# Optimization experiments

Hardware: AMD Instinct MI355X
Metric: run time of the kernel (lower is better)

## Reference

```python
import jax, jax.numpy as jnp
import numpy as np

N_HEADS, D_MODEL, D_HEAD = 16, 1024, 64
INIT_STD = 0.02


def setup_inputs() -> dict:
    key = jax.random.key(0)
    ks = jax.random.split(key, 5)
    x = jax.random.normal(ks[0], (4, 2048, D_MODEL), dtype=jnp.float32)
    W_Q = jax.random.normal(ks[1], (N_HEADS, D_MODEL, D_HEAD), dtype=jnp.float32) * INIT_STD
    W_K = jax.random.normal(ks[2], (N_HEADS, D_MODEL, D_HEAD), dtype=jnp.float32) * INIT_STD
    W_V = jax.random.normal(ks[3], (N_HEADS, D_MODEL, D_HEAD), dtype=jnp.float32) * INIT_STD
    W_O = jax.random.normal(ks[4], (N_HEADS, D_HEAD, D_MODEL), dtype=jnp.float32) * INIT_STD
    b_Q = jnp.zeros((N_HEADS, D_HEAD), dtype=jnp.float32)
    b_K = jnp.zeros((N_HEADS, D_HEAD), dtype=jnp.float32)
    b_V = jnp.zeros((N_HEADS, D_HEAD), dtype=jnp.float32)
    b_O = jnp.zeros((D_MODEL,), dtype=jnp.float32)
    return {"normalized_resid_pre": x, "W_Q": W_Q, "W_K": W_K, "W_V": W_V,
            "W_O": W_O, "b_Q": b_Q, "b_K": b_K, "b_V": b_V, "b_O": b_O}


def reference(normalized_resid_pre, W_Q, W_K, W_V, W_O, b_Q, b_K, b_V, b_O):
    x = normalized_resid_pre  # [b, s, d_model]
    q = jnp.einsum('bsm,hmd->bshd', x, W_Q) + b_Q  # [b, s, h, d_head]
    k = jnp.einsum('bsm,hmd->bshd', x, W_K) + b_K
    v = jnp.einsum('bsm,hmd->bshd', x, W_V) + b_V
    scores = jnp.einsum('bqhd,bkhd->bhqk', q, k) / jnp.sqrt(jnp.float32(D_HEAD))
    S = x.shape[1]
    causal = jnp.tril(jnp.ones((S, S), dtype=bool))  # keep key_pos <= query_pos
    scores = jnp.where(causal, scores, jnp.finfo(scores.dtype).min)
    pattern = jax.nn.softmax(scores, axis=-1)  # [b, h, q, k]
    z = jnp.einsum('bhqk,bkhd->bqhd', pattern, v)
    attn_out = jnp.einsum('bqhd,hdm->bqm', z, W_O) + b_O
    return attn_out
```

## Files before the change

### kernel.cpp

```cpp
#include <hip/hip_runtime.h>
#include <hip/hip_bf16.h>
#include <math.h>

typedef __bf16 bf16_t;
typedef bf16_t bf16x8 __attribute__((ext_vector_type(8)));
typedef float f32x4 __attribute__((ext_vector_type(4)));

#define BB 4
#define SS 2048
#define HH 16
#define DMODEL 1024
#define DHEAD 64

#define QSCALE 0.18033688011112042f

__device__ inline unsigned short f2bf(float f) {
    union { __hip_bfloat16 h; unsigned short u; } cvt;
    cvt.h = __float2bfloat16(f);
    return cvt.u;
}

__device__ __forceinline__ void gll16(const unsigned short* g, unsigned short* l) {
    __builtin_amdgcn_global_load_lds(
        (const __attribute__((address_space(1))) unsigned int*)(g),
        (__attribute__((address_space(3))) unsigned int*)(l), 16, 0, 0);
}


__global__ void pack_x(const float* __restrict__ x, unsigned short* __restrict__ xb) {
    int i = blockIdx.x * 256 + threadIdx.x;
    const float4 v = ((const float4*)x)[i];
    unsigned short o[4] = { f2bf(v.x), f2bf(v.y), f2bf(v.z), f2bf(v.w) };
    *(uint2*)(xb + 4 * (size_t)i) = *(uint2*)o;
}

__global__ void pack_wqkv(const float* __restrict__ wq, const float* __restrict__ wk,
                          const float* __restrict__ wv, unsigned short* __restrict__ out) {
    int idx = blockIdx.x * 256 + threadIdx.x;
    int k  = idx & 1023;
    int n  = idx >> 10;
    int mat = n >> 10;
    int n1 = n & 1023;
    int h = n1 >> 6, d = n1 & 63;
    const float* w = (mat == 0) ? wq : (mat == 1) ? wk : wv;
    out[idx] = f2bf(w[(h << 16) + (k << 6) + d]);
}

__global__ void pack_wo(const float* __restrict__ wo, unsigned short* __restrict__ out) {
    int idx = blockIdx.x * 256 + threadIdx.x;
    int k = idx & 1023, n = idx >> 10;
    out[idx] = f2bf(wo[(k << 10) + n]);
}


template <bool SWAP>
__device__ __forceinline__ void mf16(f32x4& d, bf16x8 a, bf16x8 b) {
    if constexpr (SWAP)
        d = __builtin_amdgcn_mfma_f32_16x16x32_bf16(b, a, d, 0, 0, 0);
    else
        d = __builtin_amdgcn_mfma_f32_16x16x32_bf16(a, b, d, 0, 0, 0);
}

#define GBAR()   __builtin_amdgcn_s_barrier()
#define SCHEDB() __builtin_amdgcn_sched_barrier(0)
#define WLGKM0() asm volatile("s_waitcnt lgkmcnt(0)" ::: "memory")

__device__ __forceinline__ void stage2(const unsigned short* g, unsigned short* lb,
                                       int T, int w) {
    const unsigned short* s = g + T * 64;
    gll16(s, lb + w * 8 * 64);
    gll16(s + 64 * 1024, lb + (64 + w * 8) * 64);
}

template <bool SWAP>
__device__ __forceinline__ void ktstep(
    unsigned short (*Ac)[64], unsigned short (*Bc)[64],
    unsigned short (*An)[64], unsigned short (*Bn)[64],
    const unsigned short* gA0, const unsigned short* gA1,
    const unsigned short* gB0, const unsigned short* gB1,
    int kt, int w, int wr, int wc, int l15, int quad, int lo,
    f32x4 (&acc)[8][4])
{
    bf16x8 a0f[4][2], a1f[4][2], bAf[2][2], bBf[2][2];
    const int c0 = (quad ^ lo) * 8;
    const int c1 = ((4 | quad) ^ lo) * 8;

#pragma unroll
    for (int mi = 0; mi < 4; mi++) {
        a0f[mi][0] = *(const bf16x8*)&Ac[wr * 128 + mi * 16 + l15][c0];
        a0f[mi][1] = *(const bf16x8*)&Ac[wr * 128 + mi * 16 + l15][c1];
    }
#pragma unroll
    for (int nj = 0; nj < 2; nj++) {
        bAf[nj][0] = *(const bf16x8*)&Bc[wc * 64 + nj * 16 + l15][c0];
        bAf[nj][1] = *(const bf16x8*)&Bc[wc * 64 + nj * 16 + l15][c1];
    }
    if (kt + 1 < 16) stage2(gB1, &Bn[128][0], kt + 1, w);
    GBAR();
    WLGKM0();
    SCHEDB();
    __builtin_amdgcn_s_setprio(1);
#pragma unroll
    for (int mi = 0; mi < 4; mi++)
#pragma unroll
        for (int nj = 0; nj < 2; nj++) {
            mf16<SWAP>(acc[mi][nj], a0f[mi][0], bAf[nj][0]);
            mf16<SWAP>(acc[mi][nj], a0f[mi][1], bAf[nj][1]);
        }
    __builtin_amdgcn_s_setprio(0);
    SCHEDB();
    GBAR();

#pragma unroll
    for (int nj = 0; nj < 2; nj++) {
        bBf[nj][0] = *(const bf16x8*)&Bc[wc * 64 + (nj + 2) * 16 + l15][c0];
        bBf[nj][1] = *(const bf16x8*)&Bc[wc * 64 + (nj + 2) * 16 + l15][c1];
    }
    if (kt + 1 < 16) stage2(gA1, &An[128][0], kt + 1, w);
    GBAR();
    WLGKM0();
    SCHEDB();
    __builtin_amdgcn_s_setprio(1);
#pragma unroll
    for (int mi = 0; mi < 4; mi++)
#pragma unroll
        for (int nj = 0; nj < 2; nj++) {
            mf16<SWAP>(acc[mi][nj + 2], a0f[mi][0], bBf[nj][0]);
            mf16<SWAP>(acc[mi][nj + 2], a0f[mi][1], bBf[nj][1]);
        }
    __builtin_amdgcn_s_setprio(0);
    SCHEDB();
    GBAR();

#pragma unroll
    for (int mi = 0; mi < 4; mi++) {
        a1f[mi][0] = *(const bf16x8*)&Ac[wr * 128 + 64 + mi * 16 + l15][c0];
        a1f[mi][1] = *(const bf16x8*)&Ac[wr * 128 + 64 + mi * 16 + l15][c1];
    }
    if (kt + 2 < 16) stage2(gB0, &Bc[0][0], kt + 2, w);
    GBAR();
    WLGKM0();
    SCHEDB();
    __builtin_amdgcn_s_setprio(1);
#pragma unroll
    for (int mi = 0; mi < 4; mi++)
#pragma unroll
        for (int nj = 0; nj < 2; nj++) {
            mf16<SWAP>(acc[4 + mi][nj + 2], a1f[mi][0], bBf[nj][0]);
            mf16<SWAP>(acc[4 + mi][nj + 2], a1f[mi][1], bBf[nj][1]);
        }
    __builtin_amdgcn_s_setprio(0);
    SCHEDB();
    GBAR();

    if (kt + 2 < 16) stage2(gA0, &Ac[0][0], kt + 2, w);
    GBAR();
    WLGKM0();
    SCHEDB();
    __builtin_amdgcn_s_setprio(1);
#pragma unroll
    for (int mi = 0; mi < 4; mi++)
#pragma unroll
        for (int nj = 0; nj < 2; nj++) {
            mf16<SWAP>(acc[4 + mi][nj], a1f[mi][0], bAf[nj][0]);
            mf16<SWAP>(acc[4 + mi][nj], a1f[mi][1], bAf[nj][1]);
        }
    __builtin_amdgcn_s_setprio(0);
    SCHEDB();
    if (kt == 14) {
        asm volatile("s_waitcnt vmcnt(0)" ::: "memory");
    } else if (kt < 14) {
        asm volatile("s_waitcnt vmcnt(4)" ::: "memory");
    }
    GBAR();
}

template <bool SWAP>
__device__ __forceinline__ void kloop256(
    unsigned short (*A0)[64], unsigned short (*A1)[64],
    unsigned short (*B0)[64], unsigned short (*B1)[64],
    const unsigned short* gA0, const unsigned short* gA1,
    const unsigned short* gB0, const unsigned short* gB1,
    int w, int wr, int wc, int l15, int quad, int lo,
    f32x4 (&acc)[8][4])
{
    stage2(gB0, &B0[0][0],   0, w);
    stage2(gA0, &A0[0][0],   0, w);
    stage2(gB1, &B0[128][0], 0, w);
    stage2(gA1, &A0[128][0], 0, w);
    stage2(gB0, &B1[0][0],   1, w);
    stage2(gA0, &A1[0][0],   1, w);
    asm volatile("s_waitcnt vmcnt(4)" ::: "memory");
    GBAR();

    for (int i = 0; i < 8; ++i) {
        ktstep<SWAP>(A0, B0, A1, B1, gA0, gA1, gB0, gB1, 2 * i,     w, wr, wc, l15, quad, lo, acc);
        ktstep<SWAP>(A1, B1, A0, B0, gA0, gA1, gB0, gB1, 2 * i + 1, w, wr, wc, l15, quad, lo, acc);
    }
}


__global__ __launch_bounds__(512, 2) void gemm_qkv8(
    const unsigned short* __restrict__ xb,
    const unsigned short* __restrict__ wT,
    const float* __restrict__ bq, const float* __restrict__ bk, const float* __restrict__ bv,
    unsigned short* __restrict__ qws, unsigned short* __restrict__ kws,
    unsigned short* __restrict__ vtw)
{
    __shared__ __align__(16) unsigned short A0s[256][64];
    __shared__ __align__(16) unsigned short A1s[256][64];
    __shared__ __align__(16) unsigned short B0s[256][64];
    __shared__ __align__(16) unsigned short B1s[256][64];

    const int t = threadIdx.x;
    const int lane = t & 63;
    const int w = t >> 6;
    const int quad = lane >> 4;
    const int l15 = lane & 15;
    const int lo = l15 & 7;
    const int wr = w >> 2;
    const int wc = w & 3;
    const int n0 = blockIdx.x * 256;
    const int m0 = blockIdx.y * 256;
    const int mat = n0 >> 10;

    const int sr8 = lane >> 3;
    const size_t soff = (size_t)(w * 8 + sr8) * 1024 + (size_t)(((lane & 7) ^ sr8) * 8);
    const unsigned short* gA0 = xb + (size_t)m0 * 1024 + soff;
    const unsigned short* gA1 = xb + (size_t)(m0 + 128) * 1024 + soff;
    const unsigned short* gB0 = wT + (size_t)n0 * 1024 + soff;
    const unsigned short* gB1 = wT + (size_t)(n0 + 128) * 1024 + soff;

    f32x4 acc[8][4] = {};

    const int b = m0 >> 11;
    const int m0r = m0 & 2047;

    if (mat != 2) {
        kloop256<true>(A0s, A1s, B0s, B1s, gA0, gA1, gB0, gB1, w, wr, wc, l15, quad, lo, acc);
        const float* bias_p = (mat == 0) ? bq : bk;
        const float scale = (mat == 0) ? QSCALE : 1.0f;
        unsigned short* dst = (mat == 0) ? qws : kws;
#pragma unroll
        for (int nj = 0; nj < 4; nj++) {
            const int noff = wc * 64 + nj * 16 + quad * 4;
            const int nmat = (n0 & 1023) + noff;
            const int h = nmat >> 6;
            const int dbase = nmat & 63;
            const float4 bv4 = *(const float4*)(bias_p + h * 64 + dbase);
            const float bias_r[4] = { bv4.x, bv4.y, bv4.z, bv4.w };
#pragma unroll
            for (int mig = 0; mig < 8; mig++) {
                const int s = m0r + wr * 128 + mig * 16 + l15;
                unsigned short pk[4];
#pragma unroll
                for (int r = 0; r < 4; r++) pk[r] = f2bf((acc[mig][nj][r] + bias_r[r]) * scale);
                *(uint2*)(dst + (size_t)((b * 16 + h) * 2048 + s) * 64 + dbase) = *(uint2*)pk;
            }
        }
    } else {
        kloop256<false>(A0s, A1s, B0s, B1s, gA0, gA1, gB0, gB1, w, wr, wc, l15, quad, lo, acc);
#pragma unroll
        for (int nj = 0; nj < 4; nj++) {
            const int n1 = (n0 & 1023) + wc * 64 + nj * 16 + l15;
            const int h = n1 >> 6, d = n1 & 63;
            const float bias = bv[h * 64 + d];
#pragma unroll
            for (int mig = 0; mig < 8; mig++) {
                const int s0 = m0r + wr * 128 + mig * 16 + quad * 4;
                unsigned short pk[4];
#pragma unroll
                for (int r = 0; r < 4; r++) pk[r] = f2bf(acc[mig][nj][r] + bias);
                *(uint2*)(vtw + ((size_t)(b * 16 + h) * 64 + d) * 2048 + s0) = *(uint2*)pk;
            }
        }
    }
}


__global__ __launch_bounds__(512, 2) void gemm_out8(
    const unsigned short* __restrict__ zb,
    const unsigned short* __restrict__ wT,
    const float* __restrict__ bo,
    float* __restrict__ out)
{
    __shared__ __align__(16) unsigned short A0s[256][64];
    __shared__ __align__(16) unsigned short A1s[256][64];
    __shared__ __align__(16) unsigned short B0s[256][64];
    __shared__ __align__(16) unsigned short B1s[256][64];

    const int t = threadIdx.x;
    const int lane = t & 63;
    const int w = t >> 6;
    const int quad = lane >> 4;
    const int l15 = lane & 15;
    const int lo = l15 & 7;
    const int wr = w >> 2;
    const int wc = w & 3;
    const int n0 = blockIdx.x * 256;
    const int m0 = blockIdx.y * 256;

    const int sr8 = lane >> 3;
    const size_t soff = (size_t)(w * 8 + sr8) * 1024 + (size_t)(((lane & 7) ^ sr8) * 8);
    const unsigned short* gA0 = zb + (size_t)m0 * 1024 + soff;
    const unsigned short* gA1 = zb + (size_t)(m0 + 128) * 1024 + soff;
    const unsigned short* gB0 = wT + (size_t)n0 * 1024 + soff;
    const unsigned short* gB1 = wT + (size_t)(n0 + 128) * 1024 + soff;

    f32x4 acc[8][4] = {};

    kloop256<true>(A0s, A1s, B0s, B1s, gA0, gA1, gB0, gB1, w, wr, wc, l15, quad, lo, acc);

#pragma unroll
    for (int nj = 0; nj < 4; nj++) {
        const int nbase = n0 + wc * 64 + nj * 16 + quad * 4;
        const float4 bv4 = *(const float4*)(bo + nbase);
#pragma unroll
        for (int mig = 0; mig < 8; mig++) {
            const int s = m0 + wr * 128 + mig * 16 + l15;
            float4 v;
            v.x = acc[mig][nj][0] + bv4.x;
            v.y = acc[mig][nj][1] + bv4.y;
            v.z = acc[mig][nj][2] + bv4.z;
            v.w = acc[mig][nj][3] + bv4.w;
            *(float4*)(out + (size_t)s * 1024 + nbase) = v;
        }
    }
}


__global__ __launch_bounds__(256) void attn3(
    const unsigned short* __restrict__ qws,
    const unsigned short* __restrict__ kws,
    const unsigned short* __restrict__ vtw,
    unsigned short* __restrict__ zb)
{
    __shared__ __align__(16) unsigned short Ks[64 * 64];
    __shared__ __align__(16) unsigned short Vs[64 * 64];
    __shared__ __align__(16) unsigned short Ps[4 * 16 * 64];

    const int t = threadIdx.x;
    const int lane = t & 63;
    const int w = t >> 6;
    const int quad = lane >> 4;
    const int l15 = lane & 15;
    const int hi = l15 >> 3;
    const int lo = l15 & 7;

    const int qt = 31 - (blockIdx.x >> 6);
    const int bh = blockIdx.x & 63;
    const int q0 = qt * 64;
    const int qbase = q0 + w * 16;
    const size_t base = (size_t)bh * SS * DHEAD;
    const unsigned short* Q = qws + base;
    const unsigned short* K = kws + base;
    const unsigned short* Vt = vtw + base;

    bf16x8 qf0 = *(const bf16x8*)(Q + (size_t)(qbase + l15) * 64 + quad * 8);
    bf16x8 qf1 = *(const bf16x8*)(Q + (size_t)(qbase + l15) * 64 + 32 + quad * 8);

    f32x4 o[4] = {};
    float lsum[4] = {0.f, 0.f, 0.f, 0.f};
    unsigned short* Pw = Ps + w * 16 * 64;

    const int sr = t >> 2;
    const int g0 = t & 3;
    const int sw0 = ((g0 ^ (sr & 7)) << 3);
    const int sw1 = (((g0 + 4) ^ (sr & 7)) << 3);
    unsigned short* ksw = Ks + sr * 64;
    unsigned short* vsw = Vs + sr * 64;
    const unsigned short* Kg = K + (size_t)sr * 64 + g0 * 8;
    const unsigned short* Vg = Vt + (size_t)sr * 2048 + g0 * 8;

    const int gq0 = ((quad ^ lo) << 3);
    const int gq1 = (((quad + 4) ^ lo) << 3);

    const int nch = qt + 1;

    uint4 kr0 = *(const uint4*)(Kg);
    uint4 kr1 = *(const uint4*)(Kg + 32);
    uint4 vr0 = *(const uint4*)(Vg);
    uint4 vr1 = *(const uint4*)(Vg + 32);

    for (int c = 0; c < nch; c++) {
        __builtin_amdgcn_sched_barrier(0);
        __builtin_amdgcn_s_barrier();
        *(uint4*)(ksw + sw0) = kr0;
        *(uint4*)(ksw + sw1) = kr1;
        *(uint4*)(vsw + sw0) = vr0;
        *(uint4*)(vsw + sw1) = vr1;
        if (c + 1 < nch) {
            const unsigned short* kp = Kg + (size_t)(c + 1) * 64 * 64;
            const unsigned short* vp = Vg + (size_t)(c + 1) * 64;
            kr0 = *(const uint4*)(kp);
            kr1 = *(const uint4*)(kp + 32);
            vr0 = *(const uint4*)(vp);
            vr1 = *(const uint4*)(vp + 32);
        }
        asm volatile("s_waitcnt lgkmcnt(0)" ::: "memory");
        __builtin_amdgcn_s_barrier();
        __builtin_amdgcn_sched_barrier(0);

        f32x4 s[4];
        __builtin_amdgcn_s_setprio(1);
#pragma unroll
        for (int sub = 0; sub < 4; sub++) {
            const unsigned short* kr = Ks + (sub * 16 + l15) * 64;
            bf16x8 kf0 = *(const bf16x8*)(kr + gq0);
            bf16x8 kf1 = *(const bf16x8*)(kr + gq1);
            f32x4 sv = {};
            sv = __builtin_amdgcn_mfma_f32_16x16x32_bf16(qf0, kf0, sv, 0, 0, 0);
            sv = __builtin_amdgcn_mfma_f32_16x16x32_bf16(qf1, kf1, sv, 0, 0, 0);
            s[sub] = sv;
        }
        __builtin_amdgcn_s_setprio(0);

        const int kb = c * 64;
        if (c == nch - 1) {
            const int qg = qbase + quad * 4;
#pragma unroll
            for (int sub = 0; sub < 4; sub++) {
                const int key = kb + sub * 16 + l15;
#pragma unroll
                for (int r = 0; r < 4; r++) {
                    float p = (key > qg + r) ? 0.f : exp2f(s[sub][r]);
                    lsum[r] += p;
                    const int q = quad * 4 + r;
                    Pw[q * 64 + (((sub * 2 + hi) ^ (q & 7)) << 3) + lo] = f2bf(p);
                }
            }
        } else {
#pragma unroll
            for (int sub = 0; sub < 4; sub++)
#pragma unroll
                for (int r = 0; r < 4; r++) {
                    float p = exp2f(s[sub][r]);
                    lsum[r] += p;
                    const int q = quad * 4 + r;
                    Pw[q * 64 + (((sub * 2 + hi) ^ (q & 7)) << 3) + lo] = f2bf(p);
                }
        }
        asm volatile("s_waitcnt lgkmcnt(0)" ::: "memory");
        bf16x8 pf0 = *(const bf16x8*)(Pw + l15 * 64 + gq0);
        bf16x8 pf1 = *(const bf16x8*)(Pw + l15 * 64 + gq1);
        __builtin_amdgcn_s_setprio(1);
#pragma unroll
        for (int dt = 0; dt < 4; dt++) {
            const unsigned short* vrp = Vs + (dt * 16 + l15) * 64;
            bf16x8 vf0 = *(const bf16x8*)(vrp + gq0);
            bf16x8 vf1 = *(const bf16x8*)(vrp + gq1);
            o[dt] = __builtin_amdgcn_mfma_f32_16x16x32_bf16(vf0, pf0, o[dt], 0, 0, 0);
            o[dt] = __builtin_amdgcn_mfma_f32_16x16x32_bf16(vf1, pf1, o[dt], 0, 0, 0);
        }
        __builtin_amdgcn_s_setprio(0);
    }

#pragma unroll
    for (int r = 0; r < 4; r++) {
        float v = lsum[r];
        v += __shfl_xor(v, 1);
        v += __shfl_xor(v, 2);
        v += __shfl_xor(v, 4);
        v += __shfl_xor(v, 8);
        lsum[r] = v;
    }
    const int srcl = (l15 >> 2) << 4;
    float t0 = __shfl(lsum[0], srcl);
    float t1 = __shfl(lsum[1], srcl);
    float t2 = __shfl(lsum[2], srcl);
    float t3 = __shfl(lsum[3], srcl);
    const int rr = l15 & 3;
    float den = (rr == 0) ? t0 : (rr == 1) ? t1 : (rr == 2) ? t2 : t3;
    const float inv = 1.0f / den;

    const int b = bh >> 4, h = bh & 15;
    const int q = qbase + l15;
    unsigned short* zrow = zb + (size_t)(b * 2048 + q) * 1024 + h * 64 + quad * 4;
#pragma unroll
    for (int dt = 0; dt < 4; dt++) {
        unsigned short pk[4];
#pragma unroll
        for (int r = 0; r < 4; r++) pk[r] = f2bf(o[dt][r] * inv);
        *(uint2*)(zrow + dt * 16) = *(uint2*)pk;
    }
}


extern "C" void kernel_launch(void* const* d_in, const int* in_sizes, int n_in,
                              void* d_out, int out_size, void* d_ws, size_t ws_size,
                              hipStream_t stream) {
    const float* x  = (const float*)d_in[0];
    const float* WQ = (const float*)d_in[1];
    const float* WK = (const float*)d_in[2];
    const float* WV = (const float*)d_in[3];
    const float* WO = (const float*)d_in[4];
    const float* bQ = (const float*)d_in[5];
    const float* bK = (const float*)d_in[6];
    const float* bV = (const float*)d_in[7];
    const float* bO = (const float*)d_in[8];
    float* out = (float*)d_out;

    char* ws = (char*)d_ws;
    unsigned short* xb   = (unsigned short*)ws;
    unsigned short* wqkv = (unsigned short*)(ws + (16u << 20));
    unsigned short* woT  = (unsigned short*)(ws + (22u << 20));
    unsigned short* qws  = (unsigned short*)(ws + (24u << 20));
    unsigned short* kws  = (unsigned short*)(ws + (40u << 20));
    unsigned short* vtw  = (unsigned short*)(ws + (56u << 20));
    unsigned short* zbuf = xb;

    pack_x<<<8192, 256, 0, stream>>>(x, xb);
    pack_wqkv<<<(3072 * 1024) / 256, 256, 0, stream>>>(WQ, WK, WV, wqkv);
    pack_wo<<<(1024 * 1024) / 256, 256, 0, stream>>>(WO, woT);
    gemm_qkv8<<<dim3(12, 32), 512, 0, stream>>>(xb, wqkv, bQ, bK, bV, qws, kws, vtw);
    attn3<<<2048, 256, 0, stream>>>(qws, kws, vtw, zbuf);
    gemm_out8<<<dim3(4, 32), 512, 0, stream>>>(zbuf, woT, bO, out);
}
```

Before: 305.8 us.

## Transpose score MFMA layout for vectorized P stores and merge pack kernels

The QK^T MFMA operands are swapped so each lane holds four consecutive keys for a single query row. That allows one packed 8-byte LDS store per 16x16 sub-tile instead of four scalar stores, and reduces the row-sum to a single accumulator finished with two cross-lane shuffles. The three fp32-to-bf16 packing kernels are merged into one launch with block-range dispatch to cut launch overhead. The new P swizzle must stay consistent with the existing read pattern, and the merged pack kernel adds some branch divergence.

New measurement: 289.4 us. 5.3% less time.

```diff
diff --git a/kernel.cpp b/kernel.cpp
--- a/kernel.cpp
+++ b/kernel.cpp
@@ -27,29 +27,31 @@
 }
 
 
-__global__ void pack_x(const float* __restrict__ x, unsigned short* __restrict__ xb) {
-    int i = blockIdx.x * 256 + threadIdx.x;
-    const float4 v = ((const float4*)x)[i];
-    unsigned short o[4] = { f2bf(v.x), f2bf(v.y), f2bf(v.z), f2bf(v.w) };
-    *(uint2*)(xb + 4 * (size_t)i) = *(uint2*)o;
-}
-
-__global__ void pack_wqkv(const float* __restrict__ wq, const float* __restrict__ wk,
-                          const float* __restrict__ wv, unsigned short* __restrict__ out) {
-    int idx = blockIdx.x * 256 + threadIdx.x;
-    int k  = idx & 1023;
-    int n  = idx >> 10;
-    int mat = n >> 10;
-    int n1 = n & 1023;
-    int h = n1 >> 6, d = n1 & 63;
-    const float* w = (mat == 0) ? wq : (mat == 1) ? wk : wv;
-    out[idx] = f2bf(w[(h << 16) + (k << 6) + d]);
-}
-
-__global__ void pack_wo(const float* __restrict__ wo, unsigned short* __restrict__ out) {
-    int idx = blockIdx.x * 256 + threadIdx.x;
-    int k = idx & 1023, n = idx >> 10;
-    out[idx] = f2bf(wo[(k << 10) + n]);
+__global__ void pack_all(const float* __restrict__ x,
+                         const float* __restrict__ wq, const float* __restrict__ wk,
+                         const float* __restrict__ wv, const float* __restrict__ wo,
+                         unsigned short* __restrict__ xb, unsigned short* __restrict__ wqkv,
+                         unsigned short* __restrict__ woT) {
+    const int bid = blockIdx.x;
+    if (bid < 8192) {
+        int i = bid * 256 + threadIdx.x;
+        const float4 v = ((const float4*)x)[i];
+        unsigned short o[4] = { f2bf(v.x), f2bf(v.y), f2bf(v.z), f2bf(v.w) };
+        *(uint2*)(xb + 4 * (size_t)i) = *(uint2*)o;
+    } else if (bid < 8192 + 12288) {
+        int idx = (bid - 8192) * 256 + threadIdx.x;
+        int k  = idx & 1023;
+        int n  = idx >> 10;
+        int mat = n >> 10;
+        int n1 = n & 1023;
+        int h = n1 >> 6, d = n1 & 63;
+        const float* wsrc = (mat == 0) ? wq : (mat == 1) ? wk : wv;
+        wqkv[idx] = f2bf(wsrc[(h << 16) + (k << 6) + d]);
+    } else {
+        int idx = (bid - 20480) * 256 + threadIdx.x;
+        int k = idx & 1023, n = idx >> 10;
+        woT[idx] = f2bf(wo[(k << 10) + n]);
+    }
 }
 
 
@@ -344,7 +346,6 @@
     const int w = t >> 6;
     const int quad = lane >> 4;
     const int l15 = lane & 15;
-    const int hi = l15 >> 3;
     const int lo = l15 & 7;
 
     const int qt = 31 - (blockIdx.x >> 6);
@@ -360,7 +361,7 @@
     bf16x8 qf1 = *(const bf16x8*)(Q + (size_t)(qbase + l15) * 64 + 32 + quad * 8);
 
     f32x4 o[4] = {};
-    float lsum[4] = {0.f, 0.f, 0.f, 0.f};
+    float lsum = 0.f;
     unsigned short* Pw = Ps + w * 16 * 64;
 
     const int sr = t >> 2;
@@ -374,6 +375,12 @@
 
     const int gq0 = ((quad ^ lo) << 3);
     const int gq1 = (((quad + 4) ^ lo) << 3);
+
+    unsigned short* pwr = Pw + l15 * 64;
+    unsigned short* pws0 = pwr + (((0 + quad) ^ (lo << 1)) << 2);
+    unsigned short* pws1 = pwr + (((4 + quad) ^ (lo << 1)) << 2);
+    unsigned short* pws2 = pwr + (((8 + quad) ^ (lo << 1)) << 2);
+    unsigned short* pws3 = pwr + (((12 + quad) ^ (lo << 1)) << 2);
 
     const int nch = qt + 1;
 
@@ -409,36 +416,41 @@
             bf16x8 kf0 = *(const bf16x8*)(kr + gq0);
             bf16x8 kf1 = *(const bf16x8*)(kr + gq1);
             f32x4 sv = {};
-            sv = __builtin_amdgcn_mfma_f32_16x16x32_bf16(qf0, kf0, sv, 0, 0, 0);
-            sv = __builtin_amdgcn_mfma_f32_16x16x32_bf16(qf1, kf1, sv, 0, 0, 0);
+            sv = __builtin_amdgcn_mfma_f32_16x16x32_bf16(kf0, qf0, sv, 0, 0, 0);
+            sv = __builtin_amdgcn_mfma_f32_16x16x32_bf16(kf1, qf1, sv, 0, 0, 0);
             s[sub] = sv;
         }
         __builtin_amdgcn_s_setprio(0);
 
         const int kb = c * 64;
         if (c == nch - 1) {
-            const int qg = qbase + quad * 4;
+            const int qg = qbase + l15;
 #pragma unroll
             for (int sub = 0; sub < 4; sub++) {
-                const int key = kb + sub * 16 + l15;
+                const int k0 = kb + sub * 16 + quad * 4;
+                unsigned short pk[4];
 #pragma unroll
                 for (int r = 0; r < 4; r++) {
-                    float p = (key > qg + r) ? 0.f : exp2f(s[sub][r]);
-                    lsum[r] += p;
-                    const int q = quad * 4 + r;
-                    Pw[q * 64 + (((sub * 2 + hi) ^ (q & 7)) << 3) + lo] = f2bf(p);
+                    float p = (k0 + r > qg) ? 0.f : exp2f(s[sub][r]);
+                    lsum += p;
+                    pk[r] = f2bf(p);
                 }
+                unsigned short* wp = (sub == 0) ? pws0 : (sub == 1) ? pws1 : (sub == 2) ? pws2 : pws3;
+                *(uint2*)wp = *(uint2*)pk;
             }
         } else {
 #pragma unroll
-            for (int sub = 0; sub < 4; sub++)
+            for (int sub = 0; sub < 4; sub++) {
+                unsigned short pk[4];
 #pragma unroll
                 for (int r = 0; r < 4; r++) {
                     float p = exp2f(s[sub][r]);
-                    lsum[r] += p;
-                    const int q = quad * 4 + r;
-                    Pw[q * 64 + (((sub * 2 + hi) ^ (q & 7)) << 3) + lo] = f2bf(p);
+                    lsum += p;
+                    pk[r] = f2bf(p);
                 }
+                unsigned short* wp = (sub == 0) ? pws0 : (sub == 1) ? pws1 : (sub == 2) ? pws2 : pws3;
+                *(uint2*)wp = *(uint2*)pk;
+            }
         }
         asm volatile("s_waitcnt lgkmcnt(0)" ::: "memory");
         bf16x8 pf0 = *(const bf16x8*)(Pw + l15 * 64 + gq0);
@@ -455,23 +467,10 @@
         __builtin_amdgcn_s_setprio(0);
     }
 
-#pragma unroll
-    for (int r = 0; r < 4; r++) {
-        float v = lsum[r];
-        v += __shfl_xor(v, 1);
-        v += __shfl_xor(v, 2);
-        v += __shfl_xor(v, 4);
-        v += __shfl_xor(v, 8);
-        lsum[r] = v;
-    }
-    const int srcl = (l15 >> 2) << 4;
-    float t0 = __shfl(lsum[0], srcl);
-    float t1 = __shfl(lsum[1], srcl);
-    float t2 = __shfl(lsum[2], srcl);
-    float t3 = __shfl(lsum[3], srcl);
-    const int rr = l15 & 3;
-    float den = (rr == 0) ? t0 : (rr == 1) ? t1 : (rr == 2) ? t2 : t3;
-    const float inv = 1.0f / den;
+    float v = lsum;
+    v += __shfl_xor(v, 16);
+    v += __shfl_xor(v, 32);
+    const float inv = 1.0f / v;
 
     const int b = bh >> 4, h = bh & 15;
     const int q = qbase + l15;
@@ -509,9 +508,7 @@
     unsigned short* vtw  = (unsigned short*)(ws + (56u << 20));
     unsigned short* zbuf = xb;
 
-    pack_x<<<8192, 256, 0, stream>>>(x, xb);
-    pack_wqkv<<<(3072 * 1024) / 256, 256, 0, stream>>>(WQ, WK, WV, wqkv);
-    pack_wo<<<(1024 * 1024) / 256, 256, 0, stream>>>(WO, woT);
+    pack_all<<<24576, 256, 0, stream>>>(x, WQ, WK, WV, WO, xb, wqkv, woT);
     gemm_qkv8<<<dim3(12, 32), 512, 0, stream>>>(xb, wqkv, bQ, bK, bV, qws, kws, vtw);
     attn3<<<2048, 256, 0, stream>>>(qws, kws, vtw, zbuf);
     gemm_out8<<<dim3(4, 32), 512, 0, stream>>>(zbuf, woT, bO, out);
```
